# Performance work log

Measured on AMD Instinct MI355X. Metric: run time of the kernel, lower is better.

Reference implementation:

```python
import jax, jax.numpy as jnp
import numpy as np

T = 5
V_TH = 0.5
GAMMA = 0.5
W_DECAY = 0.5
LOWER = 0.2 - 0.03
UPPER = 0.2 + 0.03
EMA_INIT = 0.17

@jax.custom_vjp
def sg_heaviside(x):
    return (x >= 0).astype(x.dtype)

def _sg_fwd(x):
    return sg_heaviside(x), x

def _sg_bwd(x, g):
    # grad_output * clamp(gamma - |x|, 0) / gamma^2  (triangular surrogate)
    return (g * jnp.clip(GAMMA - jnp.abs(x), 0.0) / (GAMMA * GAMMA),)

sg_heaviside.defvjp(_sg_fwd, _sg_bwd)


def setup_inputs() -> dict:
    key = jax.random.key(0)
    k1, k2 = jax.random.split(key)
    shape = (T, 32, 128, 32, 32)  # [T, B, C, H, W]
    x_exc = jax.random.uniform(k1, shape, dtype=jnp.float32)
    x_inh = jax.random.uniform(k2, shape, dtype=jnp.float32)
    alpha_raw = jnp.zeros((), dtype=jnp.float32)  # nn.Parameter alpha init 0.0
    beta_raw = jnp.zeros((), dtype=jnp.float32)   # nn.Parameter beta init 0.0
    return {"x_exc": x_exc, "x_inh": x_inh, "alpha_raw": alpha_raw, "beta_raw": beta_raw}


def reference(x_exc, x_inh, alpha_raw, beta_raw):
    beta = jax.nn.sigmoid(beta_raw)
    alpha = 4.0 * jax.nn.sigmoid(alpha_raw)
    B, C, H, W = x_exc.shape[1:]
    mem0 = jnp.zeros((B, C, H, W), x_exc.dtype)
    # ema starts constant 0.17 full-shape; after first mean it is [1,C,1,1].
    # Starting with [1,C,1,1] constant is mathematically identical.
    ema0 = jnp.full((1, C, 1, 1), EMA_INIT, x_exc.dtype)
    inhw0 = jnp.zeros((1, C, 1, 1), x_exc.dtype)

    def step(carry, xs):
        mem, ema, inhw = carry
        xe, xi = xs
        e_input = xe / (1.0 + alpha * xi)
        mem = W_DECAY * mem + e_input - beta * xi * (1.0 - inhw)
        spike = sg_heaviside(mem - V_TH)
        # ema update uses detached spikes; broadcasts [1,C,1,1]+[B,C,H,W] then means back
        ema = jnp.mean(0.9 * ema + 0.1 * jax.lax.stop_gradient(spike),
                       axis=(0, 2, 3), keepdims=True)
        # original only updates inh_weight for t < T-1, but the last update is
        # never read, so updating unconditionally is equivalent
        inhw = 4.0 * (jax.nn.sigmoid(LOWER - ema) - jax.nn.sigmoid(ema - UPPER))
        mem = mem - V_TH * spike
        return (mem, ema, inhw), spike

    _, spikes = jax.lax.scan(step, (mem0, ema0, inhw0), (x_exc, x_inh))
    return spikes  # [T, B, C, H, W]
```

## Files before the change

### kernel.cpp

```cpp
#include <hip/hip_runtime.h>

constexpr int T    = 5;
constexpr int Bn   = 32;
constexpr int C    = 128;
constexpr int HW   = 32 * 32;
constexpr int NPT4 = Bn * C * HW / 4;

constexpr int THREADS = 1024;
constexpr int WAVES   = THREADS / 64;
constexpr int F4_PER_THREAD = (Bn * HW / 4) / THREADS;

__global__ __launch_bounds__(THREADS)
void lif_kernel(const float* __restrict__ xe_g,
                const float* __restrict__ xi_g,
                const float* __restrict__ alpha_raw,
                const float* __restrict__ beta_raw,
                float* __restrict__ out) {
#pragma clang fp contract(off)
  const int c    = blockIdx.x;
  const int tid  = threadIdx.x;
  const int wave = tid >> 6;
  const int lane = tid & 63;

  __shared__ unsigned int wsum[T - 1][WAVES];

  const float alpha = 4.0f / (1.0f + expf(-alpha_raw[0]));
  const float beta  = 1.0f / (1.0f + expf(-beta_raw[0]));

  float mem[F4_PER_THREAD][4];
#pragma unroll
  for (int k = 0; k < F4_PER_THREAD; ++k)
#pragma unroll
    for (int j = 0; j < 4; ++j) mem[k][j] = 0.0f;

  float ema  = 0.17f;
  float inhw = 0.0f;

  const float4* xe4 = (const float4*)xe_g;
  const float4* xi4 = (const float4*)xi_g;
  float4*       o4  = (float4*)out;

  for (int t = 0; t < T; ++t) {
    unsigned int local = 0;
    const size_t tbase = (size_t)t * NPT4;
#pragma unroll
    for (int k = 0; k < F4_PER_THREAD; ++k) {
      const int g   = k * THREADS + tid;
      const int b   = g >> 8;
      const int off = g & 255;
      const size_t idx = tbase + (size_t)(b * C + c) * 256 + off;
      const float4 e4 = xe4[idx];
      const float4 i4 = xi4[idx];
      const float xe[4] = {e4.x, e4.y, e4.z, e4.w};
      const float xi[4] = {i4.x, i4.y, i4.z, i4.w};
      float sv[4];
#pragma unroll
      for (int j = 0; j < 4; ++j) {
        const float e_in = xe[j] / (1.0f + alpha * xi[j]);
        const float a = 0.5f * mem[k][j];
        const float bb = a + e_in;
        const float d = (beta * xi[j]) * (1.0f - inhw);
        const float m = bb - d;
        const float x = m - 0.5f;
        const float s = (x >= 0.0f) ? 1.0f : 0.0f;
        local += (x >= 0.0f) ? 1u : 0u;
        mem[k][j] = m - 0.5f * s;
        sv[j] = s;
      }
      float4 s4;
      s4.x = sv[0]; s4.y = sv[1]; s4.z = sv[2]; s4.w = sv[3];
      o4[idx] = s4;
    }

    if (t == T - 1) break;

#pragma unroll
    for (int off = 32; off > 0; off >>= 1) local += __shfl_down(local, off);
    if (lane == 0) wsum[t][wave] = local;
    __syncthreads();
    unsigned int total = 0;
#pragma unroll
    for (int w = 0; w < WAVES; ++w) total += wsum[t][w];

    const float mean_spike = (float)total * (1.0f / 32768.0f);
    ema = 0.9f * ema + 0.1f * mean_spike;
    const float s_lo = 1.0f / (1.0f + expf(-(0.17f - ema)));
    const float s_hi = 1.0f / (1.0f + expf(-(ema - 0.23f)));
    inhw = 4.0f * (s_lo - s_hi);
  }
}

extern "C" void kernel_launch(void* const* d_in, const int* in_sizes, int n_in,
                              void* d_out, int out_size, void* d_ws, size_t ws_size,
                              hipStream_t stream) {
  const float* xe = (const float*)d_in[0];
  const float* xi = (const float*)d_in[1];
  const float* ar = (const float*)d_in[2];
  const float* br = (const float*)d_in[3];
  float* out = (float*)d_out;

  lif_kernel<<<dim3(C), dim3(THREADS), 0, stream>>>(xe, xi, ar, br, out);
}
```

Baseline: 246.4 us.

## Split each channel across two blocks with a global-atomic spike-count exchange

Each channel is now handled by two blocks of 1024 threads instead of one, doubling the grid to 256 blocks so more of the device's compute units are busy. The two halves exchange per-timestep spike counts through tagged slots in the workspace, using release/acquire atomics and a spin-wait. Inputs for the next timestep are also prefetched into registers before the reduction so memory loads overlap the synchronization. The spin-wait assumes both blocks of a pair are resident at the same time and that stale tags in the workspace never match; if either assumption fails the kernel can deadlock or read a wrong count.

```diff
diff --git a/kernel.cpp b/kernel.cpp
--- a/kernel.cpp
+++ b/kernel.cpp
@@ -8,16 +8,25 @@
 
 constexpr int THREADS = 1024;
 constexpr int WAVES   = THREADS / 64;
-constexpr int F4_PER_THREAD = (Bn * HW / 4) / THREADS;
+constexpr int BLOCKS  = 2 * C;
+constexpr int F4T     = 4;
+
+constexpr unsigned int TAG0 = 0x500u;
+__device__ __forceinline__ unsigned int pack(int t, unsigned int cnt) {
+  return ((TAG0 + (unsigned)t) << 20) | cnt;
+}
 
 __global__ __launch_bounds__(THREADS)
 void lif_kernel(const float* __restrict__ xe_g,
                 const float* __restrict__ xi_g,
                 const float* __restrict__ alpha_raw,
                 const float* __restrict__ beta_raw,
-                float* __restrict__ out) {
+                float* __restrict__ out,
+                unsigned int* __restrict__ slots ) {
 #pragma clang fp contract(off)
-  const int c    = blockIdx.x;
+  const int blk  = blockIdx.x;
+  const int c    = blk & (C - 1);
+  const int half = blk >> 7;
   const int tid  = threadIdx.x;
   const int wave = tid >> 6;
   const int lane = tid & 63;
@@ -27,9 +36,9 @@
   const float alpha = 4.0f / (1.0f + expf(-alpha_raw[0]));
   const float beta  = 1.0f / (1.0f + expf(-beta_raw[0]));
 
-  float mem[F4_PER_THREAD][4];
+  float mem[F4T][4];
 #pragma unroll
-  for (int k = 0; k < F4_PER_THREAD; ++k)
+  for (int k = 0; k < F4T; ++k)
 #pragma unroll
     for (int j = 0; j < 4; ++j) mem[k][j] = 0.0f;
 
@@ -40,26 +49,35 @@
   const float4* xi4 = (const float4*)xi_g;
   float4*       o4  = (float4*)out;
 
+  auto gidx = [&](int t, int k) -> size_t {
+    const int g   = k * THREADS + tid;
+    const int b   = half * (Bn / 2) + (g >> 8);
+    const int off = g & 255;
+    return (size_t)t * NPT4 + (size_t)(b * C + c) * 256 + off;
+  };
+
+  float xe[F4T][4], xi[F4T][4];
+#pragma unroll
+  for (int k = 0; k < F4T; ++k) {
+    const size_t idx = gidx(0, k);
+    const float4 e4 = xe4[idx];
+    const float4 i4 = xi4[idx];
+    xe[k][0] = e4.x; xe[k][1] = e4.y; xe[k][2] = e4.z; xe[k][3] = e4.w;
+    xi[k][0] = i4.x; xi[k][1] = i4.y; xi[k][2] = i4.z; xi[k][3] = i4.w;
+  }
+
   for (int t = 0; t < T; ++t) {
     unsigned int local = 0;
-    const size_t tbase = (size_t)t * NPT4;
 #pragma unroll
-    for (int k = 0; k < F4_PER_THREAD; ++k) {
-      const int g   = k * THREADS + tid;
-      const int b   = g >> 8;
-      const int off = g & 255;
-      const size_t idx = tbase + (size_t)(b * C + c) * 256 + off;
-      const float4 e4 = xe4[idx];
-      const float4 i4 = xi4[idx];
-      const float xe[4] = {e4.x, e4.y, e4.z, e4.w};
-      const float xi[4] = {i4.x, i4.y, i4.z, i4.w};
+    for (int k = 0; k < F4T; ++k) {
+      const size_t idx = gidx(t, k);
       float sv[4];
 #pragma unroll
       for (int j = 0; j < 4; ++j) {
-        const float e_in = xe[j] / (1.0f + alpha * xi[j]);
+        const float e_in = xe[k][j] / (1.0f + alpha * xi[k][j]);
         const float a = 0.5f * mem[k][j];
         const float bb = a + e_in;
-        const float d = (beta * xi[j]) * (1.0f - inhw);
+        const float d = (beta * xi[k][j]) * (1.0f - inhw);
         const float m = bb - d;
         const float x = m - 0.5f;
         const float s = (x >= 0.0f) ? 1.0f : 0.0f;
@@ -75,12 +93,32 @@
     if (t == T - 1) break;
 
 #pragma unroll
+    for (int k = 0; k < F4T; ++k) {
+      const size_t idx = gidx(t + 1, k);
+      const float4 e4 = xe4[idx];
+      const float4 i4 = xi4[idx];
+      xe[k][0] = e4.x; xe[k][1] = e4.y; xe[k][2] = e4.z; xe[k][3] = e4.w;
+      xi[k][0] = i4.x; xi[k][1] = i4.y; xi[k][2] = i4.z; xi[k][3] = i4.w;
+    }
+
+#pragma unroll
     for (int off = 32; off > 0; off >>= 1) local += __shfl_down(local, off);
     if (lane == 0) wsum[t][wave] = local;
     __syncthreads();
-    unsigned int total = 0;
+    unsigned int mine = 0;
 #pragma unroll
-    for (int w = 0; w < WAVES; ++w) total += wsum[t][w];
+    for (int w = 0; w < WAVES; ++w) mine += wsum[t][w];
+
+    const int sbase = (t * C + c) * 2;
+    if (tid == 0)
+      __hip_atomic_store(&slots[sbase + half], pack(t, mine),
+                         __ATOMIC_RELEASE, __HIP_MEMORY_SCOPE_AGENT);
+    unsigned int v;
+    while (((v = __hip_atomic_load(&slots[sbase + (half ^ 1)], __ATOMIC_ACQUIRE,
+                                   __HIP_MEMORY_SCOPE_AGENT)) >> 20) !=
+           TAG0 + (unsigned)t)
+      __builtin_amdgcn_s_sleep(2);
+    const unsigned int total = mine + (v & 0xFFFFFu);
 
     const float mean_spike = (float)total * (1.0f / 32768.0f);
     ema = 0.9f * ema + 0.1f * mean_spike;
@@ -98,6 +136,7 @@
   const float* ar = (const float*)d_in[2];
   const float* br = (const float*)d_in[3];
   float* out = (float*)d_out;
+  unsigned int* slots = (unsigned int*)d_ws;
 
-  lif_kernel<<<dim3(C), dim3(THREADS), 0, stream>>>(xe, xi, ar, br, out);
+  lif_kernel<<<dim3(BLOCKS), dim3(THREADS), 0, stream>>>(xe, xi, ar, br, out, slots);
 }
```

New measurement: 436.2 us. 1.77x slower.

## Duplicate per-channel compute across two blocks to fill all CUs

Applied to the files above, without the earlier changes.

Launches two blocks per channel, each redundantly computing the full channel's membrane recurrence and spike count, while each writes only half of the outputs. This doubles the number of active blocks to occupy more compute units and hide memory latency. Loads for each timestep are also batched into registers before compute. The cost is doubled input read traffic and redundant arithmetic.

```diff
diff --git a/kernel.cpp b/kernel.cpp
--- a/kernel.cpp
+++ b/kernel.cpp
@@ -8,7 +8,8 @@
 
 constexpr int THREADS = 1024;
 constexpr int WAVES   = THREADS / 64;
-constexpr int F4_PER_THREAD = (Bn * HW / 4) / THREADS;
+constexpr int BLOCKS  = 2 * C;
+constexpr int K       = 8;
 
 __global__ __launch_bounds__(THREADS)
 void lif_kernel(const float* __restrict__ xe_g,
@@ -17,7 +18,9 @@
                 const float* __restrict__ beta_raw,
                 float* __restrict__ out) {
 #pragma clang fp contract(off)
-  const int c    = blockIdx.x;
+  const int blk  = blockIdx.x;
+  const int c    = blk & (C - 1);
+  const int half = blk >> 7;
   const int tid  = threadIdx.x;
   const int wave = tid >> 6;
   const int lane = tid & 63;
@@ -27,9 +30,9 @@
   const float alpha = 4.0f / (1.0f + expf(-alpha_raw[0]));
   const float beta  = 1.0f / (1.0f + expf(-beta_raw[0]));
 
-  float mem[F4_PER_THREAD][4];
+  float mem[K][4];
 #pragma unroll
-  for (int k = 0; k < F4_PER_THREAD; ++k)
+  for (int k = 0; k < K; ++k)
 #pragma unroll
     for (int j = 0; j < 4; ++j) mem[k][j] = 0.0f;
 
@@ -40,36 +43,45 @@
   const float4* xi4 = (const float4*)xi_g;
   float4*       o4  = (float4*)out;
 
+  auto gidx = [&](int t, int k) -> size_t {
+    const int b   = k * (THREADS / 256) + (tid >> 8);
+    const int off = tid & 255;
+    return (size_t)t * NPT4 + (size_t)(b * C + c) * 256 + off;
+  };
+
   for (int t = 0; t < T; ++t) {
+    float4 e4[K], i4[K];
+#pragma unroll
+    for (int k = 0; k < K; ++k) {
+      const size_t idx = gidx(t, k);
+      e4[k] = xe4[idx];
+      i4[k] = xi4[idx];
+    }
+
     unsigned int local = 0;
-    const size_t tbase = (size_t)t * NPT4;
 #pragma unroll
-    for (int k = 0; k < F4_PER_THREAD; ++k) {
-      const int g   = k * THREADS + tid;
-      const int b   = g >> 8;
-      const int off = g & 255;
-      const size_t idx = tbase + (size_t)(b * C + c) * 256 + off;
-      const float4 e4 = xe4[idx];
-      const float4 i4 = xi4[idx];
-      const float xe[4] = {e4.x, e4.y, e4.z, e4.w};
-      const float xi[4] = {i4.x, i4.y, i4.z, i4.w};
+    for (int k = 0; k < K; ++k) {
+      const float xe[4] = {e4[k].x, e4[k].y, e4[k].z, e4[k].w};
+      const float xi[4] = {i4[k].x, i4[k].y, i4[k].z, i4[k].w};
       float sv[4];
 #pragma unroll
       for (int j = 0; j < 4; ++j) {
         const float e_in = xe[j] / (1.0f + alpha * xi[j]);
-        const float a = 0.5f * mem[k][j];
+        const float a  = 0.5f * mem[k][j];
         const float bb = a + e_in;
-        const float d = (beta * xi[j]) * (1.0f - inhw);
-        const float m = bb - d;
-        const float x = m - 0.5f;
-        const float s = (x >= 0.0f) ? 1.0f : 0.0f;
+        const float d  = (beta * xi[j]) * (1.0f - inhw);
+        const float m  = bb - d;
+        const float x  = m - 0.5f;
+        const float s  = (x >= 0.0f) ? 1.0f : 0.0f;
         local += (x >= 0.0f) ? 1u : 0u;
         mem[k][j] = m - 0.5f * s;
         sv[j] = s;
       }
-      float4 s4;
-      s4.x = sv[0]; s4.y = sv[1]; s4.z = sv[2]; s4.w = sv[3];
-      o4[idx] = s4;
+      if ((k >> 2) == half) {
+        float4 s4;
+        s4.x = sv[0]; s4.y = sv[1]; s4.z = sv[2]; s4.w = sv[3];
+        o4[gidx(t, k)] = s4;
+      }
     }
 
     if (t == T - 1) break;
@@ -99,5 +111,5 @@
   const float* br = (const float*)d_in[3];
   float* out = (float*)d_out;
 
-  lif_kernel<<<dim3(C), dim3(THREADS), 0, stream>>>(xe, xi, ar, br, out);
+  lif_kernel<<<dim3(BLOCKS), dim3(THREADS), 0, stream>>>(xe, xi, ar, br, out);
 }
```

Measured after the change: 243.1 us. Within noise of the previous version (-1.3%).
